# Kernel tuning notes

Hardware: AMD Instinct MI355X
Metric: run time of the kernel (lower is better)

The kernel has to match this reference:

```python
import jax, jax.numpy as jnp
import numpy as np

U, I, D = 100000, 50000, 64       # users, items, latdim
H, DH = 4, 16                      # att_head, head dim (D = H*DH)
HN = 128                           # hyperNum
L = 2                              # hgnn_layer
HOPS = 2                           # gcn_hops
SLOPE = 0.5                        # leaky
NNZ_UI = 1000000
NNZ_UU = 1000000


def leaky(x):
    return jnp.where(x >= 0, x, SLOPE * x)


def spmm(rows, cols, vals, X, n_out):
    # sparse COO @ dense: out[r] += vals * X[c]
    return jax.ops.segment_sum(vals[:, None] * X[cols], rows, num_segments=n_out)


def lightgcn(uE, iE, ar, ac, av, tr, tc, tv):
    ulats, ilats = [uE], [iE]
    for _ in range(HOPS):
        tu = spmm(ar, ac, av, ilats[-1], U)
        ti = spmm(tr, tc, tv, ulats[-1], I)
        ulats.append(tu)
        ilats.append(ti)
    return sum(ulats[1:]), sum(ilats[1:])


def lightgcn2(uE, ur, uc, uv):
    lats = [uE]
    for _ in range(HOPS):
        lats.append(spmm(ur, uc, uv, lats[-1], U))
    return sum(lats[1:])


def prepare_key(E, K):
    # [N, D] -> [H, N, DH]
    return (E @ K).reshape(-1, H, DH).transpose(1, 0, 2)


def hg_transformer(E0, Key, Hyper, V, pV, W1, W2):
    # Hyper: [HN, D]; Key: [H, N, DH]
    hyp = Hyper.reshape(HN, H, DH).transpose(1, 2, 0)  # [H, DH, HN]
    total = E0
    cur = E0
    for l in range(L):
        value = (cur @ pV).reshape(-1, H, DH).transpose(1, 2, 0)   # [H, DH, N]
        t1 = ((value @ Key) @ hyp).reshape(D, HN)                  # [D, HN]
        t2 = leaky(t1 @ W1[l].T) + t1                              # Linear(HN,HN) no bias
        t3 = leaky(t2 @ W2[l].T) + t2
        pre = (t3.T @ V).reshape(HN, H, DH).transpose(1, 0, 2)     # [H, HN, DH]
        pre = hyp @ pre                                            # [H, DH, DH]
        new = (Key @ pre).transpose(1, 0, 2).reshape(-1, D)        # [N, D]
        total = total + new
        cur = new
    return total, Hyper


def setup_inputs() -> dict:
    key = jax.random.key(0)
    ks = jax.random.split(key, 14)
    s = 0.05
    uEmbeds0 = jax.random.normal(ks[0], (U, D), jnp.float32) * s
    iEmbeds0 = jax.random.normal(ks[1], (I, D), jnp.float32) * s
    Ks = jax.random.normal(ks[2], (3, D, D), jnp.float32) * (1.0 / np.sqrt(D))
    hg_Hyper = jax.random.normal(ks[3], (3, HN, D), jnp.float32) * s
    hg_V = jax.random.normal(ks[4], (3, D, D), jnp.float32) * (1.0 / np.sqrt(D))
    hg_pV = jax.random.normal(ks[5], (3, D, D), jnp.float32) * (1.0 / np.sqrt(D))
    hg_W1 = jax.random.normal(ks[6], (3, L, HN, HN), jnp.float32) * (1.0 / np.sqrt(HN))
    hg_W2 = jax.random.normal(ks[7], (3, L, HN, HN), jnp.float32) * (1.0 / np.sqrt(HN))
    adj_rows = jax.random.randint(ks[8], (NNZ_UI,), 0, U, jnp.int32)
    adj_cols = jax.random.randint(ks[9], (NNZ_UI,), 0, I, jnp.int32)
    adj_vals = jax.random.uniform(ks[10], (NNZ_UI,), jnp.float32)
    uu_rows = jax.random.randint(ks[11], (NNZ_UU,), 0, U, jnp.int32)
    uu_cols = jax.random.randint(ks[12], (NNZ_UU,), 0, U, jnp.int32)
    uu_vals = jax.random.uniform(ks[13], (NNZ_UU,), jnp.float32)
    return dict(uEmbeds0=uEmbeds0, iEmbeds0=iEmbeds0, Ks=Ks, hg_Hyper=hg_Hyper,
                hg_V=hg_V, hg_pV=hg_pV, hg_W1=hg_W1, hg_W2=hg_W2,
                adj_rows=adj_rows, adj_cols=adj_cols, adj_vals=adj_vals,
                tp_rows=adj_cols, tp_cols=adj_rows, tp_vals=adj_vals,
                uu_rows=uu_rows, uu_cols=uu_cols, uu_vals=uu_vals)


def reference(uEmbeds0, iEmbeds0, Ks, hg_Hyper, hg_V, hg_pV, hg_W1, hg_W2,
              adj_vals, tp_vals, uu_vals,
              adj_rows, adj_cols, tp_rows, tp_cols, uu_rows, uu_cols):
    ui_u_gcn, ui_i_gcn = lightgcn(uEmbeds0, iEmbeds0, adj_rows, adj_cols, adj_vals,
                                  tp_rows, tp_cols, tp_vals)
    uu_gcn = lightgcn2(uEmbeds0, uu_rows, uu_cols, uu_vals)
    ui_uEmbed0 = uEmbeds0 + ui_u_gcn
    ui_iEmbed0 = iEmbeds0 + ui_i_gcn
    uu_Embed0 = uEmbeds0 + uu_gcn
    ui_uKey = prepare_key(ui_uEmbed0, Ks[0])
    ui_iKey = prepare_key(ui_iEmbed0, Ks[1])
    uu_Key = prepare_key(uu_Embed0, Ks[2])
    ui_ulat, ui_uHyper = hg_transformer(ui_uEmbed0, ui_uKey, hg_Hyper[0], hg_V[0], hg_pV[0], hg_W1[0], hg_W2[0])
    ui_ilat, ui_iHyper = hg_transformer(ui_iEmbed0, ui_iKey, hg_Hyper[1], hg_V[1], hg_pV[1], hg_W1[1], hg_W2[1])
    uu_lat, uu_Hyper = hg_transformer(uu_Embed0, uu_Key, hg_Hyper[2], hg_V[2], hg_pV[2], hg_W1[2], hg_W2[2])
    return (ui_uEmbed0, ui_iEmbed0, ui_ulat, ui_ilat, ui_uKey, ui_iKey,
            ui_uHyper, ui_iHyper, uu_Embed0, uu_lat, uu_Key, uu_Hyper)
```

## Files before the change

### kernel.cpp

```cpp
#include <hip/hip_runtime.h>

#define ATB_B 256

__global__ __launch_bounds__(256) void hist3(const int* __restrict__ rA,
                                             const int* __restrict__ rT,
                                             const int* __restrict__ rU,
                                             int nnzA, int nnzU,
                                             int* __restrict__ cntAll, int U, int I) {
    int i = blockIdx.x * 256 + threadIdx.x;
    int tot = 2 * nnzA + nnzU;
    if (i >= tot) return;
    if (i < nnzA) atomicAdd(&cntAll[rA[i]], 1);
    else if (i < 2 * nnzA) atomicAdd(&cntAll[U + rT[i - nnzA]], 1);
    else atomicAdd(&cntAll[U + I + rU[i - 2 * nnzA]], 1);
}

__global__ __launch_bounds__(256) void scan_part3(const int* __restrict__ cntAll,
                                                  int* __restrict__ bsumAll,
                                                  int U, int I, int nbA, int nbT) {
    int b = blockIdx.x;
    int lb, n, coff, bsoff;
    if (b < nbA)            { lb = b;             n = U; coff = 0;     bsoff = 0; }
    else if (b < nbA + nbT) { lb = b - nbA;       n = I; coff = U;     bsoff = 1024; }
    else                    { lb = b - nbA - nbT; n = U; coff = U + I; bsoff = 2048; }
    __shared__ int sh[256];
    int tid = threadIdx.x;
    int i = lb * 256 + tid;
    sh[tid] = (i < n) ? cntAll[coff + i] : 0;
    __syncthreads();
    for (int st = 128; st > 0; st >>= 1) {
        if (tid < st) sh[tid] += sh[tid + st];
        __syncthreads();
    }
    if (tid == 0) bsumAll[bsoff + lb] = sh[0];
}

__global__ __launch_bounds__(1024) void scan_top3(int* __restrict__ bsumAll,
                                                  int nbA, int nbT, int nbU) {
    int g = blockIdx.x;
    int nb = (g == 0) ? nbA : (g == 1 ? nbT : nbU);
    int* b = bsumAll + g * 1024;
    __shared__ int sh[1024];
    int tid = threadIdx.x;
    int orig = (tid < nb) ? b[tid] : 0;
    sh[tid] = orig;
    __syncthreads();
    for (int st = 1; st < 1024; st <<= 1) {
        int v = (tid >= st) ? sh[tid - st] : 0;
        __syncthreads();
        sh[tid] += v;
        __syncthreads();
    }
    if (tid < nb) b[tid] = sh[tid] - orig;
}

__global__ __launch_bounds__(256) void scan_final3(int* __restrict__ curAll,
                                                   const int* __restrict__ bsumAll,
                                                   int* __restrict__ rpAll,
                                                   int U, int I, int nbA, int nbT,
                                                   int nnzA, int nnzU) {
    int b = blockIdx.x;
    int lb, n, coff, bsoff, rpoff, nnz;
    if (b < nbA)            { lb = b;             n = U; coff = 0;     bsoff = 0;    rpoff = 0;                 nnz = nnzA; }
    else if (b < nbA + nbT) { lb = b - nbA;       n = I; coff = U;     bsoff = 1024; rpoff = U + 1;             nnz = nnzA; }
    else                    { lb = b - nbA - nbT; n = U; coff = U + I; bsoff = 2048; rpoff = (U + 1) + (I + 1); nnz = nnzU; }
    __shared__ int sh[256];
    int tid = threadIdx.x;
    int i = lb * 256 + tid;
    int orig = (i < n) ? curAll[coff + i] : 0;
    sh[tid] = orig;
    __syncthreads();
    for (int st = 1; st < 256; st <<= 1) {
        int v = (tid >= st) ? sh[tid - st] : 0;
        __syncthreads();
        sh[tid] += v;
        __syncthreads();
    }
    int ex = sh[tid] - orig + bsumAll[bsoff + lb];
    if (i < n) { rpAll[rpoff + i] = ex; curAll[coff + i] = ex; }
    if (i == n - 1) rpAll[rpoff + n] = nnz;
}

__global__ __launch_bounds__(256) void scatter_r(const int* __restrict__ rows,
                                                 const int* __restrict__ cols,
                                                 const float* __restrict__ vals,
                                                 int* __restrict__ cur,
                                                 int2* __restrict__ edge,
                                                 int nnz, int w0, int wend) {
    int i = blockIdx.x * 256 + threadIdx.x;
    if (i >= nnz) return;
    int r = rows[i];
    if (r < w0 || r >= wend) return;
    int p = atomicAdd(&cur[r], 1);
    edge[p] = make_int2(cols[i], __float_as_int(vals[i]));
}

struct Seg { const int* rp; const int2* eg; const float* X; const float* a0; const float* a1; float* out; int N; };
struct Spmm3Args { Seg s0, s1, s2; int n0, n01, total; };

__global__ __launch_bounds__(256) void spmm3(Spmm3Args A) {
    int gid = blockIdx.x * 256 + threadIdx.x;
    int r = gid >> 6;
    if (r >= A.total) return;
    int d = gid & 63;
    Seg sg; int lr;
    if (r < A.n0)       { sg = A.s0; lr = r; }
    else if (r < A.n01) { sg = A.s1; lr = r - A.n0; }
    else                { sg = A.s2; lr = r - A.n01; }
    int s = sg.rp[lr], e = sg.rp[lr + 1];
    const float* __restrict__ X = sg.X;
    float acc = 0.f;
    int i = s;
    for (; i + 4 <= e; i += 4) {
        int2 e0 = sg.eg[i], e1 = sg.eg[i + 1], e2 = sg.eg[i + 2], e3 = sg.eg[i + 3];
        float x0 = X[(size_t)e0.x * 64 + d];
        float x1 = X[(size_t)e1.x * 64 + d];
        float x2 = X[(size_t)e2.x * 64 + d];
        float x3 = X[(size_t)e3.x * 64 + d];
        acc += __int_as_float(e0.y) * x0;
        acc += __int_as_float(e1.y) * x1;
        acc += __int_as_float(e2.y) * x2;
        acc += __int_as_float(e3.y) * x3;
    }
    for (; i < e; ++i) {
        int2 ee = sg.eg[i];
        acc += __int_as_float(ee.y) * X[(size_t)ee.x * 64 + d];
    }
    size_t o = (size_t)lr * 64 + d;
    if (sg.a0) acc += sg.a0[o];
    if (sg.a1) acc += sg.a1[o];
    sg.out[o] = acc;
}

struct KSeg { const float* E; const float* K; float* Kout; int N; };
struct Key3Args { KSeg s0, s1, s2; int b1, b2; };

__global__ __launch_bounds__(256) void key3(Key3Args A) {
    int b = blockIdx.x;
    KSeg sg; int lb;
    if (b >= A.b2)      { sg = A.s2; lb = b - A.b2; }
    else if (b >= A.b1) { sg = A.s1; lb = b - A.b1; }
    else                { sg = A.s0; lb = b; }
    __shared__ float Ksh[4096];
    int tid = threadIdx.x;
    for (int i = tid; i < 4096; i += 256) Ksh[i] = sg.K[i];
    __syncthreads();
    int j = tid & 63, slot = tid >> 6;
    int n = lb * 4 + slot;
    if (n >= sg.N) return;
    const float* Er = sg.E + (size_t)n * 64;
    float acc = 0.f;
#pragma unroll
    for (int kk = 0; kk < 64; ++kk) acc += Er[kk] * Ksh[kk * 64 + j];
    int h = j >> 4, dh = j & 15;
    sg.Kout[((size_t)h * sg.N + n) * 16 + dh] = acc;
}

__global__ __launch_bounds__(256) void atb3(const float* __restrict__ c0, const float* __restrict__ c1, const float* __restrict__ c2,
                                            const float* __restrict__ K0, const float* __restrict__ K1, const float* __restrict__ K2,
                                            int N0, int N1, int N2,
                                            float* __restrict__ part) {
    int kidx = blockIdx.x / ATB_B;
    int lb = blockIdx.x % ATB_B;
    const float* cur = (kidx == 0) ? c0 : (kidx == 1 ? c1 : c2);
    const float* Key = (kidx == 0) ? K0 : (kidx == 1 ? K1 : K2);
    int N = (kidx == 0) ? N0 : (kidx == 1 ? N1 : N2);
    int chunk = (N + ATB_B - 1) / ATB_B;
    int tid = threadIdx.x;
    int k = tid & 63, h = tid >> 6;
    const float* Kh = Key + (size_t)h * N * 16;
    float acc[16];
#pragma unroll
    for (int i = 0; i < 16; ++i) acc[i] = 0.f;
    int s = lb * chunk;
    int e = s + chunk;
    if (e > N) e = N;
#pragma unroll 2
    for (int n = s; n < e; ++n) {
        float c = cur[(size_t)n * 64 + k];
        const float4* kr = (const float4*)(Kh + (size_t)n * 16);
        float4 k0 = kr[0], k1 = kr[1], k2 = kr[2], k3 = kr[3];
        acc[0]  += c * k0.x;  acc[1]  += c * k0.y;  acc[2]  += c * k0.z;  acc[3]  += c * k0.w;
        acc[4]  += c * k1.x;  acc[5]  += c * k1.y;  acc[6]  += c * k1.z;  acc[7]  += c * k1.w;
        acc[8]  += c * k2.x;  acc[9]  += c * k2.y;  acc[10] += c * k2.z;  acc[11] += c * k2.w;
        acc[12] += c * k3.x;  acc[13] += c * k3.y;  acc[14] += c * k3.z;  acc[15] += c * k3.w;
    }
    float4* po = (float4*)(part + ((size_t)kidx * ATB_B + lb) * 4096 + k * 64 + h * 16);
    po[0] = make_float4(acc[0],  acc[1],  acc[2],  acc[3]);
    po[1] = make_float4(acc[4],  acc[5],  acc[6],  acc[7]);
    po[2] = make_float4(acc[8],  acc[9],  acc[10], acc[11]);
    po[3] = make_float4(acc[12], acc[13], acc[14], acc[15]);
}

__global__ __launch_bounds__(256) void reduce3(const float* __restrict__ part,
                                               float* __restrict__ Mall) {
    int k = blockIdx.x >> 4;
    int i = (blockIdx.x & 15) * 256 + threadIdx.x;
    const float* p = part + (size_t)k * ATB_B * 4096 + i;
    float s = 0.f;
#pragma unroll 8
    for (int b = 0; b < ATB_B; ++b) s += p[(size_t)b * 4096];
    Mall[k * 4096 + i] = s;
}

__global__ __launch_bounds__(1024) void chain3(const float* __restrict__ Mall,
                                               const float* __restrict__ pV,
                                               const float* __restrict__ hyp3,
                                               const float* __restrict__ W1,
                                               const float* __restrict__ W2,
                                               const float* __restrict__ Vt,
                                               float* __restrict__ pre2all, int l) {
    int kg = blockIdx.x;
    const float* M    = Mall + kg * 4096;
    const float* pVk  = pV + kg * 4096;
    const float* hyp  = hyp3 + kg * 8192;
    const float* W1kl = W1 + (size_t)(kg * 2 + l) * 16384;
    const float* W2kl = W2 + (size_t)(kg * 2 + l) * 16384;
    const float* Vk   = Vt + kg * 4096;
    float* pre2 = pre2all + kg * 1024;

    __shared__ float tA[8192];
    __shared__ float tB[8192];
    __shared__ float hypsh[8192];
    __shared__ float shW[64 * 129 + 64];
    __shared__ float VKs[1024];

    int tid = threadIdx.x;
    for (int i = tid; i < 8192; i += 1024) hypsh[i] = hyp[i];
    for (int i = tid; i < 4096; i += 1024) { shW[i] = M[i]; shW[4096 + i] = pVk[i]; }
    __syncthreads();

    {
        int d2 = tid & 15, d1 = (tid >> 4) & 15, h = tid >> 8;
        float s = 0.f;
#pragma unroll
        for (int k2 = 0; k2 < 64; ++k2)
            s += shW[4096 + k2 * 64 + h * 16 + d1] * shW[k2 * 64 + h * 16 + d2];
        VKs[tid] = s;
    }
    __syncthreads();

    for (int i = tid; i < 8192; i += 1024) {
        int m = i & 127, d = i >> 7, h = d >> 4;
        float s = 0.f;
#pragma unroll
        for (int d2 = 0; d2 < 16; ++d2) s += VKs[d * 16 + d2] * hypsh[(h * 16 + d2) * 128 + m];
        tA[i] = s;
    }
    __syncthreads();

    {
        float acc[8];
#pragma unroll
        for (int j = 0; j < 8; ++j) acc[j] = 0.f;
        for (int c = 0; c < 2; ++c) {
            __syncthreads();
            for (int t = tid; t < 8192; t += 1024) {
                int m = t >> 6, mml = t & 63;
                shW[mml * 129 + m] = W1kl[m * 128 + c * 64 + mml];
            }
            __syncthreads();
#pragma unroll
            for (int j = 0; j < 8; ++j) {
                int i = tid + j * 1024;
                int m = i & 127, d = i >> 7;
                const float* tr = tA + d * 128 + c * 64;
                float s = 0.f;
#pragma unroll
                for (int mm = 0; mm < 64; ++mm) s += tr[mm] * shW[mm * 129 + m];
                acc[j] += s;
            }
        }
#pragma unroll
        for (int j = 0; j < 8; ++j) {
            int i = tid + j * 1024;
            float s = acc[j];
            tB[i] = (s >= 0.f ? s : 0.5f * s) + tA[i];
        }
    }
    __syncthreads();

    {
        float acc[8];
#pragma unroll
        for (int j = 0; j < 8; ++j) acc[j] = 0.f;
        for (int c = 0; c < 2; ++c) {
            __syncthreads();
            for (int t = tid; t < 8192; t += 1024) {
                int m = t >> 6, mml = t & 63;
                shW[mml * 129 + m] = W2kl[m * 128 + c * 64 + mml];
            }
            __syncthreads();
#pragma unroll
            for (int j = 0; j < 8; ++j) {
                int i = tid + j * 1024;
                int m = i & 127, d = i >> 7;
                const float* tr = tB + d * 128 + c * 64;
                float s = 0.f;
#pragma unroll
                for (int mm = 0; mm < 64; ++mm) s += tr[mm] * shW[mm * 129 + m];
                acc[j] += s;
            }
        }
#pragma unroll
        for (int j = 0; j < 8; ++j) {
            int i = tid + j * 1024;
            float s = acc[j];
            tA[i] = (s >= 0.f ? s : 0.5f * s) + tB[i];
        }
    }
    __syncthreads();

    for (int i = tid; i < 4096; i += 1024) shW[i] = Vk[i];
    __syncthreads();

    for (int i = tid; i < 8192; i += 1024) {
        int dd = i & 63, m = i >> 6;
        float s = 0.f;
#pragma unroll
        for (int d = 0; d < 64; ++d) s += tA[d * 128 + m] * shW[d * 64 + dd];
        tB[i] = s;
    }
    __syncthreads();

    {
        int d2 = tid & 15, d1 = (tid >> 4) & 15, h = tid >> 8;
        float s = 0.f;
#pragma unroll
        for (int m = 0; m < 128; ++m)
            s += hypsh[(h * 16 + d1) * 128 + m] * tB[m * 64 + h * 16 + d2];
        pre2[tid] = s;
    }
}

struct ESeg { const float* Key; const float* pre2; const float* in; float* out1; float* out2; int N; };
struct Exp3Args { ESeg s0, s1, s2; int b1, b2; };

__global__ __launch_bounds__(256) void expand3(Exp3Args A, int mode) {
    int b = blockIdx.x;
    ESeg sg; int lb;
    if (b >= A.b2)      { sg = A.s2; lb = b - A.b2; }
    else if (b >= A.b1) { sg = A.s1; lb = b - A.b1; }
    else                { sg = A.s0; lb = b; }
    __shared__ float p2[1024];
    int tid = threadIdx.x;
    for (int i = tid; i < 1024; i += 256) p2[i] = sg.pre2[i];
    __syncthreads();
    int j = tid & 63, slot = tid >> 6;
    int n = lb * 4 + slot;
    if (n >= sg.N) return;
    int h = j >> 4, d2 = j & 15;
    const float* kr = sg.Key + ((size_t)h * sg.N + n) * 16;
    float s = 0.f;
#pragma unroll
    for (int d1 = 0; d1 < 16; ++d1) s += kr[d1] * p2[(h * 16 + d1) * 16 + d2];
    size_t o = (size_t)n * 64 + j;
    if (mode == 0) { sg.out1[o] = s; sg.out2[o] = sg.in[o] + s; }
    else           { sg.out1[o] = sg.in[o] + s; }
}

__global__ __launch_bounds__(256) void hyp_kernel(const float* __restrict__ Hyper,
                                                  float* __restrict__ hyp3,
                                                  float* __restrict__ out,
                                                  size_t off0, size_t off1, size_t off2) {
    int i = blockIdx.x * 256 + threadIdx.x;
    if (i >= 3 * 8192) return;
    int k = i / 8192, r = i % 8192;
    float v = Hyper[i];
    size_t off = (k == 0) ? off0 : ((k == 1) ? off1 : off2);
    out[off + r] = v;
    int m = r >> 6, dcol = r & 63;
    hyp3[k * 8192 + dcol * 128 + m] = v;
}

__global__ __launch_bounds__(256) void spmm_k(const int* __restrict__ rows,
                                              const int* __restrict__ cols,
                                              const float* __restrict__ vals,
                                              const float* __restrict__ X,
                                              float* __restrict__ out, int nnz) {
    int gid = blockIdx.x * 256 + threadIdx.x;
    int e = gid >> 6;
    if (e >= nnz) return;
    int d = gid & 63;
    int r = rows[e], c = cols[e];
    float v = vals[e];
    atomicAdd(&out[(size_t)r * 64 + d], v * X[(size_t)c * 64 + d]);
}

__global__ __launch_bounds__(256) void add3_kernel(const float* __restrict__ base,
                                                   const float* __restrict__ a,
                                                   const float* __restrict__ b,
                                                   float* __restrict__ outb, size_t n) {
    size_t i = (size_t)blockIdx.x * 256 + threadIdx.x;
    if (i >= n) return;
    outb[i] = base[i] + a[i] + b[i];
}

__global__ __launch_bounds__(256) void key_gemm(const float* __restrict__ E,
                                                const float* __restrict__ K,
                                                float* __restrict__ Kout, int N) {
    __shared__ float Ksh[4096];
    int tid = threadIdx.x;
    for (int i = tid; i < 4096; i += 256) Ksh[i] = K[i];
    __syncthreads();
    int j = tid & 63, slot = tid >> 6;
    int n = blockIdx.x * 4 + slot;
    if (n >= N) return;
    const float* Er = E + (size_t)n * 64;
    float acc = 0.f;
#pragma unroll
    for (int kk = 0; kk < 64; ++kk) acc += Er[kk] * Ksh[kk * 64 + j];
    int h = j >> 4, dh = j & 15;
    Kout[((size_t)h * N + n) * 16 + dh] = acc;
}

#define ATB_ROWS 128
__global__ __launch_bounds__(256) void atb_k(const float* __restrict__ cur,
                                             const float* __restrict__ Key,
                                             float* __restrict__ M, int N) {
    int tid = threadIdx.x;
    int k = tid & 63, h = tid >> 6;
    const float* Kh = Key + (size_t)h * N * 16;
    float acc[16];
#pragma unroll
    for (int i = 0; i < 16; ++i) acc[i] = 0.f;
    int s = blockIdx.x * ATB_ROWS;
    int e = s + ATB_ROWS;
    if (e > N) e = N;
    for (int n = s; n < e; ++n) {
        float c = cur[(size_t)n * 64 + k];
        const float4* kr = (const float4*)(Kh + (size_t)n * 16);
        float4 k0 = kr[0], k1 = kr[1], k2 = kr[2], k3 = kr[3];
        acc[0]  += c * k0.x;  acc[1]  += c * k0.y;  acc[2]  += c * k0.z;  acc[3]  += c * k0.w;
        acc[4]  += c * k1.x;  acc[5]  += c * k1.y;  acc[6]  += c * k1.z;  acc[7]  += c * k1.w;
        acc[8]  += c * k2.x;  acc[9]  += c * k2.y;  acc[10] += c * k2.z;  acc[11] += c * k2.w;
        acc[12] += c * k3.x;  acc[13] += c * k3.y;  acc[14] += c * k3.z;  acc[15] += c * k3.w;
    }
#pragma unroll
    for (int d2 = 0; d2 < 16; ++d2)
        atomicAdd(&M[k * 64 + h * 16 + d2], acc[d2]);
}

__global__ __launch_bounds__(256) void vk_small(const float* __restrict__ M,
                                                const float* __restrict__ pV,
                                                float* __restrict__ VK) {
    int i = blockIdx.x * 256 + threadIdx.x;
    if (i >= 1024) return;
    int d2 = i & 15, d1 = (i >> 4) & 15, h = i >> 8;
    float s = 0.f;
#pragma unroll
    for (int k = 0; k < 64; ++k)
        s += pV[k * 64 + h * 16 + d1] * M[k * 64 + h * 16 + d2];
    VK[i] = s;
}

__global__ __launch_bounds__(256) void t1_kernel(const float* __restrict__ VK,
                                                 const float* __restrict__ hyp,
                                                 float* __restrict__ t1) {
    int i = blockIdx.x * 256 + threadIdx.x;
    if (i >= 8192) return;
    int m = i & 127, d = i >> 7, h = d >> 4;
    float s = 0.f;
#pragma unroll
    for (int d2 = 0; d2 < 16; ++d2) s += VK[d * 16 + d2] * hyp[(h * 16 + d2) * 128 + m];
    t1[i] = s;
}

__global__ __launch_bounds__(256) void ff_kernel(const float* __restrict__ tin,
                                                 const float* __restrict__ W,
                                                 float* __restrict__ tout) {
    int i = blockIdx.x * 256 + threadIdx.x;
    if (i >= 8192) return;
    int m = i & 127, d = i >> 7;
    const float* tr = tin + d * 128;
    const float* wr = W + m * 128;
    float s = 0.f;
#pragma unroll
    for (int mm = 0; mm < 128; ++mm) s += tr[mm] * wr[mm];
    tout[i] = (s >= 0.f ? s : 0.5f * s) + tin[i];
}

__global__ __launch_bounds__(256) void pre0_kernel(const float* __restrict__ t3,
                                                   const float* __restrict__ V,
                                                   float* __restrict__ pre0) {
    int i = blockIdx.x * 256 + threadIdx.x;
    if (i >= 8192) return;
    int dd = i & 63, m = i >> 6;
    float s = 0.f;
#pragma unroll
    for (int d = 0; d < 64; ++d) s += t3[d * 128 + m] * V[d * 64 + dd];
    pre0[m * 64 + dd] = s;
}

__global__ __launch_bounds__(256) void pre2_kernel(const float* __restrict__ hyp,
                                                   const float* __restrict__ pre0,
                                                   float* __restrict__ pre2) {
    int i = blockIdx.x * 256 + threadIdx.x;
    if (i >= 1024) return;
    int d2 = i & 15, d1 = (i >> 4) & 15, h = i >> 8;
    float s = 0.f;
#pragma unroll
    for (int m = 0; m < 128; ++m) s += hyp[(h * 16 + d1) * 128 + m] * pre0[m * 64 + h * 16 + d2];
    pre2[i] = s;
}

__global__ __launch_bounds__(256) void expand0_kernel(const float* __restrict__ Key,
                                                      const float* __restrict__ pre2,
                                                      const float* __restrict__ E0,
                                                      float* __restrict__ nxt,
                                                      float* __restrict__ tot, int N) {
    __shared__ float p2[1024];
    int tid = threadIdx.x;
    for (int i = tid; i < 1024; i += 256) p2[i] = pre2[i];
    __syncthreads();
    int j = tid & 63, slot = tid >> 6;
    int n = blockIdx.x * 4 + slot;
    if (n >= N) return;
    int h = j >> 4, d2 = j & 15;
    const float* kr = Key + ((size_t)h * N + n) * 16;
    float s = 0.f;
#pragma unroll
    for (int d1 = 0; d1 < 16; ++d1) s += kr[d1] * p2[(h * 16 + d1) * 16 + d2];
    size_t o = (size_t)n * 64 + j;
    nxt[o] = s;
    tot[o] = E0[o] + s;
}

__global__ __launch_bounds__(256) void expand1_kernel(const float* __restrict__ Key,
                                                      const float* __restrict__ pre2,
                                                      const float* __restrict__ tot,
                                                      float* __restrict__ outb, int N) {
    __shared__ float p2[1024];
    int tid = threadIdx.x;
    for (int i = tid; i < 1024; i += 256) p2[i] = pre2[i];
    __syncthreads();
    int j = tid & 63, slot = tid >> 6;
    int n = blockIdx.x * 4 + slot;
    if (n >= N) return;
    int h = j >> 4, d2 = j & 15;
    const float* kr = Key + ((size_t)h * N + n) * 16;
    float s = 0.f;
#pragma unroll
    for (int d1 = 0; d1 < 16; ++d1) s += kr[d1] * p2[(h * 16 + d1) * 16 + d2];
    size_t o = (size_t)n * 64 + j;
    outb[o] = tot[o] + s;
}

extern "C" void kernel_launch(void* const* d_in, const int* in_sizes, int n_in,
                              void* d_out, int out_size, void* d_ws, size_t ws_size,
                              hipStream_t stream) {
    const float* uE      = (const float*)d_in[0];
    const float* iE      = (const float*)d_in[1];
    const float* Ks      = (const float*)d_in[2];
    const float* Hyper   = (const float*)d_in[3];
    const float* Vt      = (const float*)d_in[4];
    const float* pV      = (const float*)d_in[5];
    const float* W1      = (const float*)d_in[6];
    const float* W2      = (const float*)d_in[7];
    const int* adj_rows  = (const int*)d_in[8];
    const int* adj_cols  = (const int*)d_in[9];
    const float* adj_vals= (const float*)d_in[10];
    const int* tp_rows   = (const int*)d_in[11];
    const int* tp_cols   = (const int*)d_in[12];
    const float* tp_vals = (const float*)d_in[13];
    const int* uu_rows   = (const int*)d_in[14];
    const int* uu_cols   = (const int*)d_in[15];
    const float* uu_vals = (const float*)d_in[16];

    const int U = in_sizes[0] / 64;
    const int I = in_sizes[1] / 64;
    const int nnz_ui = in_sizes[8];
    const int nnz_uu = in_sizes[14];
    const size_t UD = (size_t)U * 64, ID = (size_t)I * 64;

    float* out = (float*)d_out;
    const size_t o_uE0 = 0;
    const size_t o_iE0 = UD;
    const size_t o_ulat = UD + ID;
    const size_t o_ilat = 2 * UD + ID;
    const size_t o_uKey = 2 * UD + 2 * ID;
    const size_t o_iKey = 3 * UD + 2 * ID;
    const size_t o_uHyp = 3 * UD + 3 * ID;
    const size_t o_iHyp = o_uHyp + 8192;
    const size_t o_uuE0 = o_iHyp + 8192;
    const size_t o_uulat = o_uuE0 + UD;
    const size_t o_uuKey = o_uulat + UD;
    const size_t o_uuHyp = o_uuKey + UD;

    float* ws   = (float*)d_ws;
    float* B1   = ws;
    float* B2   = B1 + UD;
    float* B3   = B2 + ID;
    float* Ti   = B3 + UD;
    float* Buu1 = Ti + ID;
    float* Tuu  = Buu1 + UD;
    float* hyp3 = Tuu + UD;
    float* Mall = hyp3 + 24576;
    float* pre2all = Mall + 12288;
    int2*  edge_a = (int2*)(pre2all + 3072);
    int2*  edge_t = edge_a + nnz_ui;
    int2*  edge_u = edge_t + nnz_ui;
    int*   rpAll  = (int*)(edge_u + nnz_uu);
    int*   curAll = rpAll + (U + 1) + (I + 1) + (U + 1);
    int*   bsumAll= curAll + U + I + U;
    float* partw  = (float*)(bsumAll + 3072);
    size_t need_bytes = (size_t)((char*)(partw + (size_t)3 * ATB_B * 4096) - (char*)d_ws);
    const int nbA = (U + 255) / 256, nbT = (I + 255) / 256, nbU = (U + 255) / 256;
    const bool use_new = (ws_size >= need_bytes) && (nbA <= 1024) && (nbT <= 1024);

    int* rp_a = rpAll;
    int* rp_t = rpAll + (U + 1);
    int* rp_u = rpAll + (U + 1) + (I + 1);

    if (use_new) {
        hipMemsetAsync(curAll, 0, (size_t)(U + I + U) * sizeof(int), stream);
        int totE = 2 * nnz_ui + nnz_uu;
        hist3<<<(totE + 255) / 256, 256, 0, stream>>>(adj_rows, tp_rows, uu_rows,
                                                      nnz_ui, nnz_uu, curAll, U, I);
        scan_part3<<<nbA + nbT + nbU, 256, 0, stream>>>(curAll, bsumAll, U, I, nbA, nbT);
        scan_top3<<<3, 1024, 0, stream>>>(bsumAll, nbA, nbT, nbU);
        scan_final3<<<nbA + nbT + nbU, 256, 0, stream>>>(curAll, bsumAll, rpAll,
                                                         U, I, nbA, nbT, nnz_ui, nnz_uu);
        const int gSa = (nnz_ui + 255) / 256;
        const int gSu = (nnz_uu + 255) / 256;
        const int hU = (U + 1) / 2, hI = (I + 1) / 2;
        scatter_r<<<gSa, 256, 0, stream>>>(adj_rows, adj_cols, adj_vals, curAll,         edge_a, nnz_ui, 0,  hU);
        scatter_r<<<gSa, 256, 0, stream>>>(adj_rows, adj_cols, adj_vals, curAll,         edge_a, nnz_ui, hU, U);
        scatter_r<<<gSa, 256, 0, stream>>>(tp_rows,  tp_cols,  tp_vals,  curAll + U,     edge_t, nnz_ui, 0,  hI);
        scatter_r<<<gSa, 256, 0, stream>>>(tp_rows,  tp_cols,  tp_vals,  curAll + U,     edge_t, nnz_ui, hI, I);
        scatter_r<<<gSu, 256, 0, stream>>>(uu_rows,  uu_cols,  uu_vals,  curAll + U + I, edge_u, nnz_uu, 0,  hU);
        scatter_r<<<gSu, 256, 0, stream>>>(uu_rows,  uu_cols,  uu_vals,  curAll + U + I, edge_u, nnz_uu, hU, U);

        {
            Spmm3Args A;
            A.s0 = { rp_t, edge_t, uE, nullptr, nullptr, B2, I };
            A.s1 = { rp_a, edge_a, iE, nullptr, nullptr, B1, U };
            A.s2 = { nullptr, nullptr, nullptr, nullptr, nullptr, nullptr, 0 };
            A.n0 = I; A.n01 = I + U; A.total = I + U;
            spmm3<<<(int)(((size_t)A.total * 64 + 255) / 256), 256, 0, stream>>>(A);
        }
        {
            Spmm3Args A;
            A.s0 = { rp_a, edge_a, B2, uE, B1, out + o_uE0, U };
            A.s1 = { rp_t, edge_t, B1, iE, B2, out + o_iE0, I };
            A.s2 = { rp_u, edge_u, uE, nullptr, nullptr, Buu1, U };
            A.n0 = U; A.n01 = U + I; A.total = U + I + U;
            spmm3<<<(int)(((size_t)A.total * 64 + 255) / 256), 256, 0, stream>>>(A);
        }
        {
            Spmm3Args A;
            A.s0 = { rp_u, edge_u, Buu1, uE, Buu1, out + o_uuE0, U };
            A.s1 = { nullptr, nullptr, nullptr, nullptr, nullptr, nullptr, 0 };
            A.s2 = A.s1;
            A.n0 = U; A.n01 = U; A.total = U;
            spmm3<<<(int)(((size_t)A.total * 64 + 255) / 256), 256, 0, stream>>>(A);
        }

        hyp_kernel<<<(3 * 8192 + 255) / 256, 256, 0, stream>>>(Hyper, hyp3, out,
                                                               o_uHyp, o_iHyp, o_uuHyp);

        const int gb0 = (U + 3) / 4, gb1 = (I + 3) / 4, gb2 = (U + 3) / 4;
        {
            Key3Args A;
            A.s0 = { out + o_uE0,  Ks,        out + o_uKey,  U };
            A.s1 = { out + o_iE0,  Ks + 4096, out + o_iKey,  I };
            A.s2 = { out + o_uuE0, Ks + 8192, out + o_uuKey, U };
            A.b1 = gb0; A.b2 = gb0 + gb1;
            key3<<<gb0 + gb1 + gb2, 256, 0, stream>>>(A);
        }

        const float* Key0 = out + o_uKey;
        const float* Key1 = out + o_iKey;
        const float* Key2 = out + o_uuKey;

        for (int l = 0; l < 2; ++l) {
            const float* c0 = (l == 0) ? (out + o_uE0)  : B1;
            const float* c1 = (l == 0) ? (out + o_iE0)  : B2;
            const float* c2 = (l == 0) ? (out + o_uuE0) : Buu1;

            atb3<<<3 * ATB_B, 256, 0, stream>>>(c0, c1, c2, Key0, Key1, Key2, U, I, U, partw);
            reduce3<<<48, 256, 0, stream>>>(partw, Mall);
            chain3<<<3, 1024, 0, stream>>>(Mall, pV, hyp3, W1, W2, Vt, pre2all, l);

            Exp3Args E;
            E.b1 = gb0; E.b2 = gb0 + gb1;
            if (l == 0) {
                E.s0 = { Key0, pre2all,        out + o_uE0,  B1,   B3,  U };
                E.s1 = { Key1, pre2all + 1024, out + o_iE0,  B2,   Ti,  I };
                E.s2 = { Key2, pre2all + 2048, out + o_uuE0, Buu1, Tuu, U };
                expand3<<<gb0 + gb1 + gb2, 256, 0, stream>>>(E, 0);
            } else {
                E.s0 = { Key0, pre2all,        B3,  out + o_ulat,  nullptr, U };
                E.s1 = { Key1, pre2all + 1024, Ti,  out + o_ilat,  nullptr, I };
                E.s2 = { Key2, pre2all + 2048, Tuu, out + o_uulat, nullptr, U };
                expand3<<<gb0 + gb1 + gb2, 256, 0, stream>>>(E, 1);
            }
        }
    } else {
        float* fB1 = ws;
        float* fB2 = fB1 + UD;
        float* fB3 = fB2 + ID;
        float* fhyp3 = fB2;
        float* fVK  = fhyp3 + 3 * 8192;
        float* ft1  = fVK + 1024;
        float* ft2  = ft1 + 8192;
        float* ft3  = ft2 + 8192;
        float* fpre0 = ft3 + 8192;
        float* fpre2 = fpre0 + 8192;
        float* fM   = fpre2 + 1024;

        const int g_ui = (int)(((size_t)nnz_ui * 64 + 255) / 256);
        const int g_uu = (int)(((size_t)nnz_uu * 64 + 255) / 256);
        const int gU = (int)((UD + 255) / 256);
        const int gI = (int)((ID + 255) / 256);
        hipMemsetAsync(fB1, 0, UD * sizeof(float), stream);
        spmm_k<<<g_ui, 256, 0, stream>>>(adj_rows, adj_cols, adj_vals, iE, fB1, nnz_ui);
        hipMemsetAsync(fB2, 0, ID * sizeof(float), stream);
        spmm_k<<<g_ui, 256, 0, stream>>>(tp_rows, tp_cols, tp_vals, uE, fB2, nnz_ui);
        hipMemsetAsync(fB3, 0, UD * sizeof(float), stream);
        spmm_k<<<g_ui, 256, 0, stream>>>(adj_rows, adj_cols, adj_vals, fB2, fB3, nnz_ui);
        add3_kernel<<<gU, 256, 0, stream>>>(uE, fB1, fB3, out + o_uE0, UD);
        hipMemsetAsync(fB3, 0, ID * sizeof(float), stream);
        spmm_k<<<g_ui, 256, 0, stream>>>(tp_rows, tp_cols, tp_vals, fB1, fB3, nnz_ui);
        add3_kernel<<<gI, 256, 0, stream>>>(iE, fB2, fB3, out + o_iE0, ID);
        hipMemsetAsync(fB1, 0, UD * sizeof(float), stream);
        spmm_k<<<g_uu, 256, 0, stream>>>(uu_rows, uu_cols, uu_vals, uE, fB1, nnz_uu);
        hipMemsetAsync(fB3, 0, UD * sizeof(float), stream);
        spmm_k<<<g_uu, 256, 0, stream>>>(uu_rows, uu_cols, uu_vals, fB1, fB3, nnz_uu);
        add3_kernel<<<gU, 256, 0, stream>>>(uE, fB1, fB3, out + o_uuE0, UD);

        hyp_kernel<<<(3 * 8192 + 255) / 256, 256, 0, stream>>>(Hyper, fhyp3, out,
                                                               o_uHyp, o_iHyp, o_uuHyp);

        const int    Narr[3] = { U, I, U };
        const size_t oE[3]   = { o_uE0, o_iE0, o_uuE0 };
        const size_t oK[3]   = { o_uKey, o_iKey, o_uuKey };
        const size_t oL[3]   = { o_ulat, o_ilat, o_uulat };

        for (int k = 0; k < 3; ++k) {
            int N = Narr[k];
            const float* E0k = out + oE[k];
            float* Keyk = out + oK[k];
            const float* Ksk = Ks + k * 4096;
            const float* pVk = pV + k * 4096;
            const float* Vk  = Vt + k * 4096;
            const float* hypk = fhyp3 + k * 8192;

            key_gemm<<<(N + 3) / 4, 256, 0, stream>>>(E0k, Ksk, Keyk, N);

            for (int l = 0; l < 2; ++l) {
                const float* W1kl = W1 + (size_t)(k * 2 + l) * 16384;
                const float* W2kl = W2 + (size_t)(k * 2 + l) * 16384;

                hipMemsetAsync(fM, 0, 4096 * sizeof(float), stream);
                atb_k<<<(N + ATB_ROWS - 1) / ATB_ROWS, 256, 0, stream>>>(
                    (l == 0) ? E0k : fB1, Keyk, fM, N);
                vk_small<<<4, 256, 0, stream>>>(fM, pVk, fVK);
                t1_kernel<<<32, 256, 0, stream>>>(fVK, hypk, ft1);
                ff_kernel<<<32, 256, 0, stream>>>(ft1, W1kl, ft2);
                ff_kernel<<<32, 256, 0, stream>>>(ft2, W2kl, ft3);
                pre0_kernel<<<32, 256, 0, stream>>>(ft3, Vk, fpre0);
                pre2_kernel<<<4, 256, 0, stream>>>(hypk, fpre0, fpre2);

                if (l == 0) {
                    expand0_kernel<<<(N + 3) / 4, 256, 0, stream>>>(Keyk, fpre2, E0k, fB1, fB3, N);
                } else {
                    expand1_kernel<<<(N + 3) / 4, 256, 0, stream>>>(Keyk, fpre2, fB3, out + oL[k], N);
                }
            }
        }
    }
}
```

Baseline: 1.640 ms.

## Make key projection persistent with per-wavefront row ranges and register-held K

The key3 kernel changes from one block per four rows, each staging the 64x64 K matrix into shared memory, to a persistent grid of 2048 blocks. Each 64-lane wavefront walks a contiguous range of rows across the three segments and keeps its K column in 64 registers, reloading only when the segment changes. This removes the per-block shared-memory staging, the barrier and the launch overhead of many small blocks. In exchange it raises register pressure, may lower occupancy, and makes row reads wavefront-uniform scalar loads.

```diff
diff --git a/kernel.cpp b/kernel.cpp
--- a/kernel.cpp
+++ b/kernel.cpp
@@ -133,27 +133,35 @@
 }
 
 struct KSeg { const float* E; const float* K; float* Kout; int N; };
-struct Key3Args { KSeg s0, s1, s2; int b1, b2; };
+struct Key3Args { KSeg s0, s1, s2; int n0, n01, total; };
 
 __global__ __launch_bounds__(256) void key3(Key3Args A) {
-    int b = blockIdx.x;
-    KSeg sg; int lb;
-    if (b >= A.b2)      { sg = A.s2; lb = b - A.b2; }
-    else if (b >= A.b1) { sg = A.s1; lb = b - A.b1; }
-    else                { sg = A.s0; lb = b; }
-    __shared__ float Ksh[4096];
-    int tid = threadIdx.x;
-    for (int i = tid; i < 4096; i += 256) Ksh[i] = sg.K[i];
-    __syncthreads();
-    int j = tid & 63, slot = tid >> 6;
-    int n = lb * 4 + slot;
-    if (n >= sg.N) return;
-    const float* Er = sg.E + (size_t)n * 64;
-    float acc = 0.f;
-#pragma unroll
-    for (int kk = 0; kk < 64; ++kk) acc += Er[kk] * Ksh[kk * 64 + j];
-    int h = j >> 4, dh = j & 15;
-    sg.Kout[((size_t)h * sg.N + n) * 16 + dh] = acc;
+    int nw = (gridDim.x * 256) >> 6;
+    int w  = (blockIdx.x * 256 + threadIdx.x) >> 6;
+    int j  = threadIdx.x & 63;
+    int chunk = (A.total + nw - 1) / nw;
+    int r0 = w * chunk;
+    int r1 = r0 + chunk; if (r1 > A.total) r1 = A.total;
+
+    float Kreg[64];
+    int curseg = -1;
+    for (int r = r0; r < r1; ++r) {
+        int seg = (r < A.n0) ? 0 : ((r < A.n01) ? 1 : 2);
+        KSeg sg = (seg == 0) ? A.s0 : ((seg == 1) ? A.s1 : A.s2);
+        int lr = r - ((seg == 0) ? 0 : ((seg == 1) ? A.n0 : A.n01));
+        if (seg != curseg) {
+            curseg = seg;
+#pragma unroll
+            for (int kk = 0; kk < 64; ++kk) Kreg[kk] = sg.K[kk * 64 + j];
+        }
+        int nu = __builtin_amdgcn_readfirstlane(lr);
+        const float* Er = sg.E + (size_t)nu * 64;
+        float acc = 0.f;
+#pragma unroll
+        for (int kk = 0; kk < 64; ++kk) acc += Er[kk] * Kreg[kk];
+        int h = j >> 4, dh = j & 15;
+        sg.Kout[((size_t)h * sg.N + nu) * 16 + dh] = acc;
+    }
 }
 
 __global__ __launch_bounds__(256) void atb3(const float* __restrict__ c0, const float* __restrict__ c1, const float* __restrict__ c2,
@@ -659,19 +667,19 @@
         hyp_kernel<<<(3 * 8192 + 255) / 256, 256, 0, stream>>>(Hyper, hyp3, out,
                                                                o_uHyp, o_iHyp, o_uuHyp);
 
-        const int gb0 = (U + 3) / 4, gb1 = (I + 3) / 4, gb2 = (U + 3) / 4;
         {
             Key3Args A;
             A.s0 = { out + o_uE0,  Ks,        out + o_uKey,  U };
             A.s1 = { out + o_iE0,  Ks + 4096, out + o_iKey,  I };
             A.s2 = { out + o_uuE0, Ks + 8192, out + o_uuKey, U };
-            A.b1 = gb0; A.b2 = gb0 + gb1;
-            key3<<<gb0 + gb1 + gb2, 256, 0, stream>>>(A);
+            A.n0 = U; A.n01 = U + I; A.total = U + I + U;
+            key3<<<2048, 256, 0, stream>>>(A);
         }
 
         const float* Key0 = out + o_uKey;
         const float* Key1 = out + o_iKey;
         const float* Key2 = out + o_uuKey;
+        const int gb0 = (U + 3) / 4, gb1 = (I + 3) / 4, gb2 = (U + 3) / 4;
 
         for (int l = 0; l < 2; ++l) {
             const float* c0 = (l == 0) ? (out + o_uE0)  : B1;
```

Result: no change. 1.615 ms (-1.5%).
